# Optimization experiments

Measured on AMD Instinct MI355X. Metric: run time of the kernel, lower is better.

## Reference

```python
import jax, jax.numpy as jnp
import numpy as np
from jax import lax

# LNS semantics: values are held as (sign, log_base|x|); exact conversion round-trips
# make log-domain mul/add mathematically identical to float conv/linear/relu, so the
# faithful reference is the equivalent float pipeline.

def _conv(x, w, b):
    # x: [B,C,H,W], w: [O,C,kh,kw] (torch layout), stride 1, no padding
    y = lax.conv_general_dilated(x, w, window_strides=(1, 1), padding='VALID',
                                 dimension_numbers=('NCHW', 'OIHW', 'NCHW'))
    return y + b[None, :, None, None]

def _maxpool2(x):
    return lax.reduce_window(x, -jnp.inf, lax.max,
                             window_dimensions=(1, 1, 2, 2),
                             window_strides=(1, 1, 2, 2), padding='VALID')

def setup_inputs() -> dict:
    key = jax.random.key(0)
    ks = jax.random.split(key, 9)
    s = lambda k, shape, fan: jax.random.normal(k, shape, jnp.float32) * (1.0 / np.sqrt(fan))
    return {
        'x': jax.random.normal(ks[0], (512, 1, 54, 54), jnp.float32),
        'conv1_w': s(ks[1], (32, 1, 3, 3), 9),
        'conv1_b': s(ks[2], (32,), 9),
        'conv2_w': s(ks[3], (64, 32, 3, 3), 32 * 9),
        'conv2_b': s(ks[4], (64,), 32 * 9),
        'fc1_w': s(ks[5], (128, 9216), 9216),
        'fc1_b': s(ks[6], (128,), 9216),
        'fc2_w': s(ks[7], (10, 128), 128),
        'fc2_b': s(ks[8], (10,), 128),
    }

def reference(x, conv1_w, conv1_b, conv2_w, conv2_b, fc1_w, fc1_b, fc2_w, fc2_b):
    h = jnp.maximum(_conv(x, conv1_w, conv1_b), 0.0)          # [B,32,52,52]
    h = _maxpool2(h)                                          # [B,32,26,26]
    h = jnp.maximum(_conv(h, conv2_w, conv2_b), 0.0)          # [B,64,24,24]
    h = _maxpool2(h)                                          # [B,64,12,12]
    h = h.reshape(h.shape[0], -1)                             # [B,9216]
    h = jnp.maximum(h @ fc1_w.T + fc1_b, 0.0)                 # [B,128]
    return h @ fc2_w.T + fc2_b                                # [B,10]
```

## Files before the change

kernel.cpp:

```cpp
#include <hip/hip_runtime.h>


#define B 512
#define POS 676
#define ICP 36
#define P2SZ (64*12*12)
#define SCR 26
#define IMS 58
#define IMCOPY (54 * IMS)
#define PL_USH (POS * ICP)
#define SCRATCH_USH 6656

typedef unsigned short ushort_t;
typedef ushort_t ushort4v __attribute__((ext_vector_type(4)));
typedef _Float16 f16x8 __attribute__((ext_vector_type(8)));
typedef float f32x4 __attribute__((ext_vector_type(4)));

__device__ __forceinline__ ushort_t f2h(float f) {
    union { _Float16 h; ushort_t u; } a; a.h = (_Float16)f; return a.u;
}
__device__ __forceinline__ float h2f(ushort_t u) {
    union { ushort_t u; _Float16 h; } a; a.u = u; return (float)a.h;
}

#define N_WR (64 * 9 * 32)
#define WR_BLOCKS 72
#define TR_BLOCKS 128

__global__ __launch_bounds__(256) void prep(const float* __restrict__ c2w,
                                            const float* __restrict__ f1w,
                                            ushort_t* __restrict__ wr,
                                            ushort_t* __restrict__ wfb) {
    __shared__ float tr[64 * 145];
    int blk = blockIdx.x;
    int tid = threadIdx.x;

    if (blk < WR_BLOCKS) {
        int t = blk * 256 + tid;
        int ic  = t & 31;
        int tap = (t >> 5) % 9;
        int oc  = t / 288;
        wr[t] = f2h(c2w[oc * 288 + ic * 9 + tap]);
        return;
    }
    int n = blk - WR_BLOCKS;
    const float* src = f1w + (size_t)n * 9216;
#pragma unroll
    for (int i = 0; i < 36; ++i) {
        int idx = i * 256 + tid;
        int oc = idx / 144, pos = idx - oc * 144;
        tr[oc * 145 + pos] = src[idx];
    }
    __syncthreads();
    ushort_t* dst = wfb + (size_t)n * 9216;
#pragma unroll
    for (int i = 0; i < 36; ++i) {
        int idx = i * 256 + tid;
        int pos = idx >> 6, oc = idx & 63;
        dst[idx] = f2h(tr[oc * 145 + pos]);
    }
}

__global__ __launch_bounds__(512, 4) void conv12(const float* __restrict__ x,
                                                 const float* __restrict__ w1,
                                                 const float* __restrict__ bias1,
                                                 const ushort_t* __restrict__ wr,
                                                 const float* __restrict__ bias2,
                                                 ushort_t* __restrict__ pool2cl) {
    __shared__ ushort_t smem[PL_USH + SCRATCH_USH];
    ushort_t* pl  = smem;
    ushort_t* img = smem + PL_USH;

    int b   = blockIdx.x;
    int tid = threadIdx.x;
    int lane = tid & 63, wid = tid >> 6;
    int quad = lane >> 4, lr = lane & 15;

    for (int i = tid; i < 54; i += 512) {
        ushort_t* r0 = img + i * IMS;
        r0[54] = 0; r0[55] = 0; r0[56] = 0; r0[57] = 0;
        ushort_t* r1 = img + IMCOPY + i * IMS;
        r1[53] = 0; r1[54] = 0; r1[55] = 0; r1[56] = 0; r1[57] = 0;
    }
    if (tid < 96) img[2 * IMCOPY + tid] = 0;

    const float* xim = x + (size_t)b * 2916;
    for (int i = tid; i < 2916; i += 512) {
        int r = i / 54, c = i - r * 54;
        ushort_t v = f2h(xim[i]);
        img[r * IMS + c] = v;
        if (c > 0) img[IMCOPY + r * IMS + c - 1] = v;
    }

    f16x8 bfrag[2];
#pragma unroll
    for (int n = 0; n < 2; ++n) {
        union { ushort_t u[8]; f16x8 v; } bu;
#pragma unroll
        for (int j = 0; j < 8; ++j) bu.u[j] = 0;
        if (quad < 3) {
            const float* wp = w1 + (n * 16 + lr) * 9 + quad * 3;
            bu.u[0] = f2h(wp[0]);
            bu.u[1] = f2h(wp[1]);
            bu.u[2] = f2h(wp[2]);
        }
        bfrag[n] = bu.v;
    }
    float bv0 = bias1[lr], bv1 = bias1[16 + lr];

    __syncthreads();

    int cbase = (lr & 1) ? (IMCOPY + lr - 1) : lr;

    for (int it = 0; it < 4; ++it) {
        int py = wid + it * 8;
        if (py >= 26) break;
        int y0 = 2 * py;
#pragma unroll
        for (int t = 0; t < 4; ++t) {
            int x0 = t * 16;
            int off0 = cbase + x0 + (y0 + quad) * IMS;
            int off1 = off0 + IMS;
            union { unsigned d[4]; f16x8 v; } a0, a1;
            a0.d[0] = *reinterpret_cast<const unsigned*>(&img[off0]);
            a0.d[1] = *reinterpret_cast<const unsigned*>(&img[off0 + 2]);
            a0.d[2] = a0.d[0]; a0.d[3] = a0.d[1];
            a1.d[0] = *reinterpret_cast<const unsigned*>(&img[off1]);
            a1.d[1] = *reinterpret_cast<const unsigned*>(&img[off1 + 2]);
            a1.d[2] = a1.d[0]; a1.d[3] = a1.d[1];

            f32x4 cA0 = (f32x4){0.f,0.f,0.f,0.f}, cA1 = cA0, cB0 = cA0, cB1 = cA0;
            cA0 = __builtin_amdgcn_mfma_f32_16x16x32_f16(a0.v, bfrag[0], cA0, 0, 0, 0);
            cA1 = __builtin_amdgcn_mfma_f32_16x16x32_f16(a0.v, bfrag[1], cA1, 0, 0, 0);
            cB0 = __builtin_amdgcn_mfma_f32_16x16x32_f16(a1.v, bfrag[0], cB0, 0, 0, 0);
            cB1 = __builtin_amdgcn_mfma_f32_16x16x32_f16(a1.v, bfrag[1], cB1, 0, 0, 0);

            if (t < 3 || quad == 0) {
                int px0 = t * 8 + quad * 2;
                float u0 = fmaxf(fmaxf(cA0[0], cA0[1]), fmaxf(cB0[0], cB0[1]));
                float u1 = fmaxf(fmaxf(cA0[2], cA0[3]), fmaxf(cB0[2], cB0[3]));
                float v0 = fmaxf(fmaxf(cA1[0], cA1[1]), fmaxf(cB1[0], cB1[1]));
                float v1 = fmaxf(fmaxf(cA1[2], cA1[3]), fmaxf(cB1[2], cB1[3]));
                ushort_t* po = pl + (py * 26 + px0) * ICP;
                po[lr]            = f2h(fmaxf(u0 + bv0, 0.0f));
                po[16 + lr]       = f2h(fmaxf(v0 + bv1, 0.0f));
                po[ICP + lr]      = f2h(fmaxf(u1 + bv0, 0.0f));
                po[ICP + 16 + lr] = f2h(fmaxf(v1 + bv1, 0.0f));
            }
        }
    }

    __syncthreads();

    int prow  = wid >> 1;
    int nhalf = wid & 1;
    const ushort_t* wb = wr + (size_t)(nhalf * 32 + lr) * 288 + quad * 8;

    int ocl = lane & 31;
    int pxh = lane >> 5;
    int oc  = nhalf * 32 + ocl;
    float bv = bias2[oc];
    ushort_t* scr = smem + PL_USH + wid * (32 * SCR);

    for (int cc = 0; cc < 3; ++cc) {
        int ebase[3];
#pragma unroll
        for (int t = 0; t < 3; ++t) {
            int m  = t * 16 + lr;
            int yl = m / 24;
            int xx = m - yl * 24;
            ebase[t] = ((8 * cc + 2 * prow + yl) * 26 + xx) * ICP + quad * 8;
        }

        f32x4 acc[3][2];
#pragma unroll
        for (int t = 0; t < 3; ++t)
#pragma unroll
            for (int n = 0; n < 2; ++n) acc[t][n] = (f32x4){0.f, 0.f, 0.f, 0.f};

#pragma unroll
        for (int tap = 0; tap < 9; ++tap) {
            int ky = tap / 3, kx = tap % 3;
            int koff = (ky * 26 + kx) * ICP;
            f16x8 a[3];
#pragma unroll
            for (int t = 0; t < 3; ++t) {
                union { ushort4v s[2]; f16x8 v; } u;
                u.s[0] = *reinterpret_cast<const ushort4v*>(&pl[ebase[t] + koff]);
                u.s[1] = *reinterpret_cast<const ushort4v*>(&pl[ebase[t] + koff + 4]);
                a[t] = u.v;
            }
            f16x8 bf[2];
#pragma unroll
            for (int n = 0; n < 2; ++n)
                bf[n] = *reinterpret_cast<const f16x8*>(wb + (size_t)n * 16 * 288 + tap * 32);
#pragma unroll
            for (int t = 0; t < 3; ++t)
#pragma unroll
                for (int n = 0; n < 2; ++n)
                    acc[t][n] = __builtin_amdgcn_mfma_f32_16x16x32_f16(a[t], bf[n], acc[t][n], 0, 0, 0);
        }

#pragma unroll
        for (int t = 0; t < 3; ++t)
#pragma unroll
            for (int n = 0; n < 2; ++n) {
                int wocl = n * 16 + lr;
                int i0 = t * 8 + quad * 2;
                float v0 = fmaxf(acc[t][n][0], acc[t][n][1]);
                float v1 = fmaxf(acc[t][n][2], acc[t][n][3]);
                union { ushort_t u2[2]; unsigned w; } pk;
                pk.u2[0] = f2h(v0); pk.u2[1] = f2h(v1);
                *reinterpret_cast<unsigned*>(&scr[wocl * SCR + i0]) = pk.w;
            }
        __syncthreads();

        const ushort_t* row = scr + ocl * SCR;
        int py = cc * 4 + prow;
        ushort_t* po = pool2cl + ((size_t)b * 144 + py * 12) * 64 + oc;
#pragma unroll
        for (int j = 0; j < 6; ++j) {
            int px = pxh * 6 + j;
            float r0 = h2f(row[px]);
            float r1 = h2f(row[px + 12]);
            po[px * 64] = f2h(fmaxf(fmaxf(r0, r1) + bv, 0.0f));
        }
    }
}

__global__ __launch_bounds__(256) void fc1_mfma(const ushort_t* __restrict__ A,
                                                 const ushort_t* __restrict__ W,
                                                 float* __restrict__ Cpart) {
    int tid = threadIdx.x;
    int lane = tid & 63, wid = tid >> 6;
    int lr = lane & 15, quad = lane >> 4;
    int w  = blockIdx.x * 4 + wid;
    int nt = w & 3;
    int ks = (w >> 2) & 15;
    int mt = w >> 6;

    int m0 = mt * 16;
    int n0 = nt * 32;
    int k0 = ks * 576 + quad * 8;
    const ushort_t* a0 = A + (size_t)(m0 + lr) * 9216 + k0;
    const ushort_t* b0 = W + (size_t)(n0 + lr) * 9216 + k0;
    const ushort_t* b1 = b0 + (size_t)16 * 9216;

    f32x4 acc0 = (f32x4){0.f, 0.f, 0.f, 0.f};
    f32x4 acc1 = (f32x4){0.f, 0.f, 0.f, 0.f};

#pragma unroll
    for (int kk = 0; kk < 18; ++kk) {
        f16x8 av  = *reinterpret_cast<const f16x8*>(a0 + kk * 32);
        f16x8 bv0 = *reinterpret_cast<const f16x8*>(b0 + kk * 32);
        f16x8 bv1 = *reinterpret_cast<const f16x8*>(b1 + kk * 32);
        acc0 = __builtin_amdgcn_mfma_f32_16x16x32_f16(av, bv0, acc0, 0, 0, 0);
        acc1 = __builtin_amdgcn_mfma_f32_16x16x32_f16(av, bv1, acc1, 0, 0, 0);
    }

    float* cp = Cpart + (size_t)ks * (512 * 128);
    int crow = m0 + quad * 4;
#pragma unroll
    for (int r = 0; r < 4; ++r) {
        cp[(size_t)(crow + r) * 128 + n0 + lr]      = acc0[r];
        cp[(size_t)(crow + r) * 128 + n0 + 16 + lr] = acc1[r];
    }
}

__global__ __launch_bounds__(256) void fc1fc2(const float* __restrict__ Cpart,
                                              const float* __restrict__ b1,
                                              const float* __restrict__ w2,
                                              const float* __restrict__ b2,
                                              float* __restrict__ out) {
    __shared__ float h[2][128];
    int half = threadIdx.x >> 7;
    int k = threadIdx.x & 127;
    int b = blockIdx.x * 2 + half;
    float s = 0.f;
#pragma unroll
    for (int ks = 0; ks < 16; ++ks) s += Cpart[(size_t)ks * (512 * 128) + b * 128 + k];
    h[half][k] = fmaxf(s + b1[k], 0.0f);
    __syncthreads();
    if (k < 10) {
        const float* wp = w2 + k * 128;
        float acc = 0.f;
#pragma unroll 8
        for (int j = 0; j < 128; ++j) acc += h[half][j] * wp[j];
        out[b * 10 + k] = acc + b2[k];
    }
}

extern "C" void kernel_launch(void* const* d_in, const int* in_sizes, int n_in,
                              void* d_out, int out_size, void* d_ws, size_t ws_size,
                              hipStream_t stream) {
    const float* x       = (const float*)d_in[0];
    const float* conv1_w = (const float*)d_in[1];
    const float* conv1_b = (const float*)d_in[2];
    const float* conv2_w = (const float*)d_in[3];
    const float* conv2_b = (const float*)d_in[4];
    const float* fc1_w   = (const float*)d_in[5];
    const float* fc1_b   = (const float*)d_in[6];
    const float* fc2_w   = (const float*)d_in[7];
    const float* fc2_b   = (const float*)d_in[8];
    float* out = (float*)d_out;

    char* ws = (char*)d_ws;
    ushort_t* wr = (ushort_t*)ws;
    ws += N_WR * sizeof(ushort_t) + 128;
    ushort_t* wfb = (ushort_t*)ws;
    ws += (size_t)128 * 9216 * sizeof(ushort_t) + 128;
    ushort_t* pool2cl = (ushort_t*)ws;
    ws += (size_t)B * P2SZ * sizeof(ushort_t) + 128;
    float* Cpart = (float*)ws;
    ws += (size_t)16 * 512 * 128 * sizeof(float) + 128;

    prep<<<WR_BLOCKS + TR_BLOCKS, 256, 0, stream>>>(conv2_w, fc1_w, wr, wfb);
    conv12<<<B, 512, 0, stream>>>(x, conv1_w, conv1_b, wr, conv2_b, pool2cl);
    fc1_mfma<<<512, 256, 0, stream>>>(pool2cl, wfb, Cpart);
    fc1fc2<<<256, 256, 0, stream>>>(Cpart, fc1_b, fc2_w, fc2_b, out);
}
```

Measured before the change: 119.3 us.

## Fuse fc1 MFMA GEMM with bias, ReLU and fc2 in one kernel

Replaces the split-K fc1 MFMA kernel and the separate reduction plus fc2 kernel with a single kernel. Each block owns 16 batch rows and reduces over K with two wave halves, combining partials in shared memory before applying bias, ReLU and fc2. This removes the global Cpart partial buffer round trip and one kernel launch. The cost is a grid of only 32 blocks with long serial K loops, which leaves most CUs idle and makes each wave latency-bound.

```diff
diff --git a/kernel.cpp b/kernel.cpp
--- a/kernel.cpp
+++ b/kernel.cpp
@@ -26,6 +26,7 @@
 #define N_WR (64 * 9 * 32)
 #define WR_BLOCKS 72
 #define TR_BLOCKS 128
+#define FC_BLOCKS 32
 
 __global__ __launch_bounds__(256) void prep(const float* __restrict__ c2w,
                                             const float* __restrict__ f1w,
@@ -228,65 +229,69 @@
     }
 }
 
-__global__ __launch_bounds__(256) void fc1_mfma(const ushort_t* __restrict__ A,
-                                                 const ushort_t* __restrict__ W,
-                                                 float* __restrict__ Cpart) {
-    int tid = threadIdx.x;
+__global__ __launch_bounds__(512) void fc12(const ushort_t* __restrict__ A,
+                                            const ushort_t* __restrict__ W,
+                                            const float* __restrict__ fb1,
+                                            const float* __restrict__ w2,
+                                            const float* __restrict__ fb2,
+                                            float* __restrict__ out) {
+    __shared__ float part[2][16][128];
+    __shared__ float w2s[10 * 128];
+    int tid  = threadIdx.x;
     int lane = tid & 63, wid = tid >> 6;
-    int lr = lane & 15, quad = lane >> 4;
-    int w  = blockIdx.x * 4 + wid;
-    int nt = w & 3;
-    int ks = (w >> 2) & 15;
-    int mt = w >> 6;
-
-    int m0 = mt * 16;
-    int n0 = nt * 32;
-    int k0 = ks * 576 + quad * 8;
-    const ushort_t* a0 = A + (size_t)(m0 + lr) * 9216 + k0;
-    const ushort_t* b0 = W + (size_t)(n0 + lr) * 9216 + k0;
-    const ushort_t* b1 = b0 + (size_t)16 * 9216;
+    int lr   = lane & 15, quad = lane >> 4;
+    int kh   = wid >> 2;
+    int nt   = wid & 3;
+    int m0   = blockIdx.x * 16;
+    int n0   = nt * 32;
+    int k0   = kh * 4608;
+
+    for (int i = tid; i < 1280; i += 512) w2s[i] = w2[i];
+
+    const ushort_t* a0  = A + (size_t)(m0 + lr) * 9216 + k0 + quad * 8;
+    const ushort_t* b0  = W + (size_t)(n0 + lr) * 9216 + k0 + quad * 8;
+    const ushort_t* b1p = b0 + (size_t)16 * 9216;
 
     f32x4 acc0 = (f32x4){0.f, 0.f, 0.f, 0.f};
     f32x4 acc1 = (f32x4){0.f, 0.f, 0.f, 0.f};
 
-#pragma unroll
-    for (int kk = 0; kk < 18; ++kk) {
+#pragma unroll 4
+    for (int kk = 0; kk < 144; ++kk) {
         f16x8 av  = *reinterpret_cast<const f16x8*>(a0 + kk * 32);
         f16x8 bv0 = *reinterpret_cast<const f16x8*>(b0 + kk * 32);
-        f16x8 bv1 = *reinterpret_cast<const f16x8*>(b1 + kk * 32);
+        f16x8 bv1 = *reinterpret_cast<const f16x8*>(b1p + kk * 32);
         acc0 = __builtin_amdgcn_mfma_f32_16x16x32_f16(av, bv0, acc0, 0, 0, 0);
         acc1 = __builtin_amdgcn_mfma_f32_16x16x32_f16(av, bv1, acc1, 0, 0, 0);
     }
 
-    float* cp = Cpart + (size_t)ks * (512 * 128);
-    int crow = m0 + quad * 4;
+    int mrow = quad * 4;
 #pragma unroll
     for (int r = 0; r < 4; ++r) {
-        cp[(size_t)(crow + r) * 128 + n0 + lr]      = acc0[r];
-        cp[(size_t)(crow + r) * 128 + n0 + 16 + lr] = acc1[r];
-    }
-}
-
-__global__ __launch_bounds__(256) void fc1fc2(const float* __restrict__ Cpart,
-                                              const float* __restrict__ b1,
-                                              const float* __restrict__ w2,
-                                              const float* __restrict__ b2,
-                                              float* __restrict__ out) {
-    __shared__ float h[2][128];
-    int half = threadIdx.x >> 7;
-    int k = threadIdx.x & 127;
-    int b = blockIdx.x * 2 + half;
-    float s = 0.f;
-#pragma unroll
-    for (int ks = 0; ks < 16; ++ks) s += Cpart[(size_t)ks * (512 * 128) + b * 128 + k];
-    h[half][k] = fmaxf(s + b1[k], 0.0f);
-    __syncthreads();
-    if (k < 10) {
-        const float* wp = w2 + k * 128;
+        part[kh][mrow + r][n0 + lr]      = acc0[r];
+        part[kh][mrow + r][n0 + 16 + lr] = acc1[r];
+    }
+    __syncthreads();
+
+    {
+        int idx = tid * 4;
+        int r = idx >> 7, c = idx & 127;
+        f32x4 p0 = *reinterpret_cast<const f32x4*>(&part[0][r][c]);
+        f32x4 p1 = *reinterpret_cast<const f32x4*>(&part[1][r][c]);
+        f32x4 bb = *reinterpret_cast<const f32x4*>(&fb1[c]);
+#pragma unroll
+        for (int j = 0; j < 4; ++j) p0[j] = fmaxf(p0[j] + p1[j] + bb[j], 0.0f);
+        *reinterpret_cast<f32x4*>(&part[0][r][c]) = p0;
+    }
+    __syncthreads();
+
+    if (tid < 160) {
+        int r = tid & 15, o = tid >> 4;
+        const float* hp = &part[0][r][0];
+        const float* wp = &w2s[o * 128];
         float acc = 0.f;
 #pragma unroll 8
-        for (int j = 0; j < 128; ++j) acc += h[half][j] * wp[j];
-        out[b * 10 + k] = acc + b2[k];
+        for (int j = 0; j < 128; ++j) acc += hp[j] * wp[j];
+        out[(m0 + r) * 10 + o] = acc + fb2[o];
     }
 }
 
@@ -311,11 +316,8 @@
     ws += (size_t)128 * 9216 * sizeof(ushort_t) + 128;
     ushort_t* pool2cl = (ushort_t*)ws;
     ws += (size_t)B * P2SZ * sizeof(ushort_t) + 128;
-    float* Cpart = (float*)ws;
-    ws += (size_t)16 * 512 * 128 * sizeof(float) + 128;
 
     prep<<<WR_BLOCKS + TR_BLOCKS, 256, 0, stream>>>(conv2_w, fc1_w, wr, wfb);
     conv12<<<B, 512, 0, stream>>>(x, conv1_w, conv1_b, wr, conv2_b, pool2cl);
-    fc1_mfma<<<512, 256, 0, stream>>>(pool2cl, wfb, Cpart);
-    fc1fc2<<<256, 256, 0, stream>>>(Cpart, fc1_b, fc2_w, fc2_b, out);
-}
+    fc12<<<FC_BLOCKS, 512, 0, stream>>>(pool2cl, wfb, fc1_b, fc2_w, fc2_b, out);
+}
```

New measurement: 196.6 us. +64.8%, slower.
